# Optimization experiments

Hardware: AMD Instinct MI355X
Metric: run time of the kernel (lower is better)

## Reference

```python
import jax, jax.numpy as jnp
import numpy as np
from jax import lax

# 5x5 ring kernel: all ones except center (same_class_neighbor in the torch code)
_RING = np.ones((5, 5), dtype=np.float32)
_RING[2, 2] = 0.0


def _ring_dwconv(x, channels):
    """Depthwise 5x5 'ring' conv, padding=2 (groups=channels in torch)."""
    k = jnp.broadcast_to(jnp.asarray(_RING)[None, None], (channels, 1, 5, 5))
    return lax.conv_general_dilated(
        x, k, window_strides=(1, 1), padding='SAME',
        dimension_numbers=('NCHW', 'OIHW', 'NCHW'),
        feature_group_count=channels)


def _gt2boundary(gt, ignore_label=-1, bw=5):
    # gt: [B,H,W] int. Differences over a width-5 offset, padded back to size.
    ud = jnp.pad(gt[:, bw:, :] - gt[:, :-bw, :], ((0, 0), (0, bw), (0, 0))) != 0
    lr = jnp.pad(gt[:, :, bw:] - gt[:, :, :-bw], ((0, 0), (0, 0), (0, bw))) != 0
    return ud | lr | (gt == ignore_label)


def setup_inputs() -> dict:
    key = jax.random.key(0)
    k1, k2, k3 = jax.random.split(key, 3)
    B, C, H, W, NC = 4, 256, 256, 256, 2
    out_features = jax.random.normal(k1, (B, C, H, W), dtype=jnp.float32)
    out_classifier = jax.random.normal(k2, (B, NC, H, W), dtype=jnp.float32)
    gt_sem = jax.random.randint(k3, (B, H, W), 0, 2)
    return {"out_features": out_features, "out_classifier": out_classifier, "gt_sem": gt_sem}


def reference(out_features, out_classifier, gt_sem):
    NUM_CLASSES = 2
    B, C, H, W = out_features.shape
    # boundary mask (gt2boundary); interpolation to er_input size is identity here
    edge = _gt2boundary(gt_sem)  # [B,H,W] bool
    pred = jnp.argmax(out_classifier, axis=1)  # [B,H,W]

    total = jnp.float32(0.0)
    ncls = jnp.float32(0.0)
    for c in range(NUM_CLASSES):
        cm = (gt_sem == c).astype(out_features.dtype)   # now_class_mask
        pm = (pred == c).astype(out_features.dtype)     # now_pred_class_mask
        corr = cm * pm                                   # correctly-predicted class mask
        # depthwise ring-neighborhood sums
        neigh_feat = _ring_dwconv(out_features * corr[:, None], C)      # [B,C,H,W]
        cnt_class = _ring_dwconv(cm[:, None], 1)[:, 0]                  # [B,H,W]
        cnt_corr = _ring_dwconv(corr[:, None], 1)[:, 0]                 # [B,H,W]
        cal_mask = (cnt_class >= 1) & edge & (cm > 0)
        mse_mask = (cnt_corr >= 1) & edge & (cm > 0) & (pm > 0)
        # mean neighbor feature of correctly-predicted same-class neighbors
        feat = neigh_feat / (cnt_corr[:, None] + 1e-5)
        m = mse_mask.astype(out_features.dtype)
        nsel = jnp.sum(m)
        diff = (out_features - lax.stop_gradient(feat)) * m[:, None]
        # F.mse_loss(reduction='mean') over selected pixels x C channels
        loss_c = jnp.sum(diff * diff) / jnp.maximum(nsel * C, 1.0)
        valid = (jnp.sum(cal_mask) >= 1) & (jnp.sum(mse_mask) >= 1)
        total = total + jnp.where(valid, loss_c, 0.0)
        ncls = ncls + valid.astype(jnp.float32)
    # if no class contributed, return 0 (the unaveraged total); else average
    return jnp.where(ncls == 0, total, total / jnp.maximum(ncls, 1.0))
```

## Files before the change

kernel.cpp:

```cpp
#include <hip/hip_runtime.h>
#include <stdint.h>

#define BB 4
#define CC 256
#define HH 256
#define WW 256
#define TH 16
#define TR 20
#define NCH 8
#define NTILES (HH/TH)
#define NCHUNKS (CC/NCH)

__global__ void k_init(unsigned int* p) {
    if (threadIdx.x < 8) p[threadIdx.x] = 0;
}

__global__ void k_code(const float* __restrict__ cls, const int* __restrict__ gt,
                       unsigned char* __restrict__ code) {
    int i = blockIdx.x * 256 + threadIdx.x;
    int w = i & 255, h = (i >> 8) & 255;
    int b = i >> 16;
    int g = gt[i];
    float c0 = cls[((b*2 + 0)*HH + h)*WW + w];
    float c1 = cls[((b*2 + 1)*HH + h)*WW + w];
    int pred = (c1 > c0) ? 1 : 0;
    int ud = (h < HH-5) ? (gt[i + 5*WW] != g) : 0;
    int lr = (w < WW-5) ? (gt[i + 5] != g) : 0;
    int edge = (ud | lr | (g == -1)) ? 1 : 0;
    int lab = (g == 0) ? 0 : ((g == 1) ? 1 : 2);
    int good = (lab < 2 && pred == g) ? 1 : 0;
    code[i] = (unsigned char)(lab | (good << 2) | (edge << 3));
}

__device__ __forceinline__ float f4get(const float4& v, int j) {
    switch (j) { case 0: return v.x; case 1: return v.y; case 2: return v.z; default: return v.w; }
}

__device__ __forceinline__ void hwin_f(const float* vs, float* S, int l) {
    float eL0 = __shfl(vs[2], l - 1, 64);
    float eL1 = __shfl(vs[3], l - 1, 64);
    float eR0 = __shfl(vs[0], l + 1, 64);
    float eR1 = __shfl(vs[1], l + 1, 64);
    if (l == 0)  { eL0 = 0.f; eL1 = 0.f; }
    if (l == 63) { eR0 = 0.f; eR1 = 0.f; }
    float m = vs[1] + vs[2];
    float core = vs[0] + m;
    float c2 = m + vs[3];
    S[0] = core + eL0 + eL1;
    S[1] = core + vs[3] + eL1;
    S[2] = core + vs[3] + eR0;
    S[3] = c2 + eR0 + eR1;
}

__device__ __forceinline__ void hwin_i(const int* vs, int* S, int l) {
    int eL0 = __shfl(vs[2], l - 1, 64);
    int eL1 = __shfl(vs[3], l - 1, 64);
    int eR0 = __shfl(vs[0], l + 1, 64);
    int eR1 = __shfl(vs[1], l + 1, 64);
    if (l == 0)  { eL0 = 0; eL1 = 0; }
    if (l == 63) { eR0 = 0; eR1 = 0; }
    int m = vs[1] + vs[2];
    int core = vs[0] + m;
    int c2 = m + vs[3];
    S[0] = core + eL0 + eL1;
    S[1] = core + vs[3] + eL1;
    S[2] = core + vs[3] + eR0;
    S[3] = c2 + eR0 + eR1;
}

__global__ __launch_bounds__(256) void k_loss(const float* __restrict__ F,
                                              const unsigned char* __restrict__ code,
                                              double* __restrict__ lsum,
                                              unsigned int* __restrict__ cnts) {
    __shared__ unsigned int csh[TR*64];
    __shared__ float red[8];
    const int t = threadIdx.x, w = t >> 6, l = t & 63;
    const int bx = blockIdx.x;
    const int chunk = bx & (NCHUNKS - 1);
    const int tile = (bx >> 5) & (NTILES - 1);
    const int b = bx >> 9;
    const int R0 = tile * TH;

    for (int idx = t; idx < TR*64; idx += 256) {
        int rr = idx >> 6, grow = R0 - 2 + rr;
        unsigned int v = 0x02020202u;
        if ((unsigned)grow < HH) v = ((const unsigned int*)code)[(b*HH + grow)*64 + (idx & 63)];
        csh[idx] = v;
    }
    __syncthreads();

    const int rbase = R0 + 4*w - 2;

    unsigned int cw[8];
    #pragma unroll
    for (int rr = 0; rr < 8; rr++) cw[rr] = csh[(4*w + rr)*64 + l];

    float fm0[8][4], fm1[8][4];
    unsigned int mgd[8], mcls[8];
    #pragma unroll
    for (int rr = 0; rr < 8; rr++) {
        unsigned int u = cw[rr], mg = 0, mc = 0;
        #pragma unroll
        for (int j = 0; j < 4; j++) {
            unsigned int q = (u >> (8*j)) & 255u;
            unsigned int lab2 = q & 3u, good = (q >> 2) & 1u;
            unsigned int c0 = (lab2 == 0u) ? 1u : 0u;
            unsigned int c1 = (lab2 == 1u) ? 1u : 0u;
            mg |= (c0 & good) << j;
            mg |= (c1 & good) << (4 + j);
            mc |= c0 << j;
            mc |= c1 << (4 + j);
            fm0[rr][j] = (float)(c0 & good);
            fm1[rr][j] = (float)(c1 & good);
        }
        mgd[rr] = mg; mcls[rr] = mc;
    }

    float wq[16];
    unsigned int mse0bits = 0, mse1bits = 0, labbits = 0;
    int ccal0 = 0, ccal1 = 0, cms0 = 0, cms1 = 0;
    #pragma unroll
    for (int o = 0; o < 4; o++) {
        int vg0[4] = {0,0,0,0}, vg1[4] = {0,0,0,0}, vc0[4] = {0,0,0,0}, vc1[4] = {0,0,0,0};
        #pragma unroll
        for (int k = 0; k < 5; k++) {
            unsigned int mg = mgd[o+k], mc = mcls[o+k];
            #pragma unroll
            for (int j = 0; j < 4; j++) {
                vg0[j] += (mg >> j) & 1;  vg1[j] += (mg >> (4+j)) & 1;
                vc0[j] += (mc >> j) & 1;  vc1[j] += (mc >> (4+j)) & 1;
            }
        }
        int bg0[4], bg1[4], bc0[4], bc1[4];
        hwin_i(vg0, bg0, l); hwin_i(vg1, bg1, l);
        hwin_i(vc0, bc0, l); hwin_i(vc1, bc1, l);
        #pragma unroll
        for (int j = 0; j < 4; j++) {
            unsigned int q = (cw[o+2] >> (8*j)) & 255u;
            int lab2 = q & 3, good = (q >> 2) & 1, edge = (q >> 3) & 1;
            int bcl = (lab2 == 1) ? bc1[j] : bc0[j];
            int bgl = (lab2 == 1) ? bg1[j] : bg0[j];
            int ccls = bcl - 1;
            int ccorr = bgl - good;
            int isc = (lab2 < 2) && edge;
            int cal = isc && (ccls >= 1);
            int mse = isc && good && (ccorr >= 1);
            int idx = o*4 + j;
            wq[idx] = mse ? (1.0f / ((float)ccorr + 1e-5f)) : 0.0f;
            labbits  |= ((unsigned)(lab2 & 1)) << idx;
            mse0bits |= ((unsigned)(mse & (lab2 == 0))) << idx;
            mse1bits |= ((unsigned)(mse & (lab2 == 1))) << idx;
            ccal0 += cal & (lab2 == 0);  ccal1 += cal & (lab2 == 1);
            cms0  += mse & (lab2 == 0);  cms1  += mse & (lab2 == 1);
        }
    }

    if (chunk == 0) {
        for (int off = 32; off > 0; off >>= 1) {
            ccal0 += __shfl_down(ccal0, off, 64);
            ccal1 += __shfl_down(ccal1, off, 64);
            cms0  += __shfl_down(cms0,  off, 64);
            cms1  += __shfl_down(cms1,  off, 64);
        }
        if (l == 0) {
            atomicAdd(&cnts[0], (unsigned)ccal0);
            atomicAdd(&cnts[1], (unsigned)ccal1);
            atomicAdd(&cnts[2], (unsigned)cms0);
            atomicAdd(&cnts[3], (unsigned)cms1);
        }
    }

    unsigned int rowok = 0;
    #pragma unroll
    for (int rr = 0; rr < 8; rr++)
        if ((unsigned)(rbase + rr) < HH) rowok |= 1u << rr;

    const float4* fb = (const float4*)F + (((size_t)(b*CC + chunk*NCH)) << 14);
    float acc0 = 0.f, acc1 = 0.f;

    #pragma unroll 1
    for (int c = 0; c < NCH; c++) {
        const float4* pl = fb + ((size_t)c << 14);
        float4 ring[5];
        #pragma unroll
        for (int rr = 0; rr < 8; rr++) {
            float4 v = make_float4(0.f, 0.f, 0.f, 0.f);
            if (rowok & (1u << rr)) v = pl[(rbase + rr)*64 + l];
            ring[rr % 5] = v;
            if (rr >= 4) {
                const int o = rr - 4;
                float vs0[4] = {0.f,0.f,0.f,0.f}, vs1[4] = {0.f,0.f,0.f,0.f};
                #pragma unroll
                for (int k = 0; k < 5; k++) {
                    const int row = o + k;
                    const float4 rv = ring[row % 5];
                    #pragma unroll
                    for (int j = 0; j < 4; j++) {
                        float x = f4get(rv, j);
                        vs0[j] = fmaf(fm0[row][j], x, vs0[j]);
                        vs1[j] = fmaf(fm1[row][j], x, vs1[j]);
                    }
                }
                float S0[4], S1[4];
                hwin_f(vs0, S0, l);
                hwin_f(vs1, S1, l);
                const float4 ctr = ring[(o + 2) % 5];
                #pragma unroll
                for (int j = 0; j < 4; j++) {
                    const int idx = o*4 + j;
                    float fc = f4get(ctr, j);
                    float Ssel = ((labbits >> idx) & 1u) ? S1[j] : S0[j];
                    float S = Ssel - fc;
                    float d = fmaf(-S, wq[idx], fc);
                    float dd = d * d;
                    acc0 += ((mse0bits >> idx) & 1u) ? dd : 0.f;
                    acc1 += ((mse1bits >> idx) & 1u) ? dd : 0.f;
                }
            }
        }
    }

    for (int off = 32; off > 0; off >>= 1) {
        acc0 += __shfl_down(acc0, off, 64);
        acc1 += __shfl_down(acc1, off, 64);
    }
    if (l == 0) { red[w*2] = acc0; red[w*2 + 1] = acc1; }
    __syncthreads();
    if (t == 0) {
        float a0 = red[0] + red[2] + red[4] + red[6];
        float a1 = red[1] + red[3] + red[5] + red[7];
        atomicAdd(&lsum[0], (double)a0);
        atomicAdd(&lsum[1], (double)a1);
    }
}

__global__ void k_final(const double* __restrict__ lsum,
                        const unsigned int* __restrict__ cnts, float* out) {
    if (threadIdx.x == 0 && blockIdx.x == 0) {
        float total = 0.f, ncls = 0.f;
        for (int c = 0; c < 2; c++) {
            double num = lsum[c];
            unsigned int calc = cnts[c], msec = cnts[2 + c];
            float denom = fmaxf((float)msec * (float)CC, 1.0f);
            float lc = (float)(num / (double)denom);
            if (calc >= 1u && msec >= 1u) { total += lc; ncls += 1.f; }
        }
        out[0] = (ncls == 0.f) ? total : total / fmaxf(ncls, 1.f);
    }
}

extern "C" void kernel_launch(void* const* d_in, const int* in_sizes, int n_in,
                              void* d_out, int out_size, void* d_ws, size_t ws_size,
                              hipStream_t stream) {
    const float* feats = (const float*)d_in[0];
    const float* cls   = (const float*)d_in[1];
    const int*   gt    = (const int*)d_in[2];
    double* lsum = (double*)d_ws;
    unsigned int* cnts = (unsigned int*)((char*)d_ws + 16);
    unsigned char* code = (unsigned char*)d_ws + 64;
    float* out = (float*)d_out;

    const int npix = BB*HH*WW;
    k_init<<<1, 64, 0, stream>>>((unsigned int*)d_ws);
    k_code<<<npix/256, 256, 0, stream>>>(cls, gt, code);
    k_loss<<<BB*NTILES*NCHUNKS, 256, 0, stream>>>(feats, code, lsum, cnts);
    k_final<<<1, 64, 0, stream>>>(lsum, cnts, out);
}
```

Before: 444.1 us.

## Double-buffer channel row loads and use DPP row shifts for horizontal window

The channel loop now prefetches the next channel's 8 rows into a second register buffer while the current one is computed, so global load latency overlaps compute. Cross-lane neighbor exchange switches from __shfl to DPP wave_shl/wave_shr with bound_ctrl zero-fill, which removes the ds_bpermute and the edge-lane masking. Launch bounds now request 3 waves per SIMD, and fewer code words are kept in registers. The extra float4 buffers raise register pressure, which may cause spills or lower occupancy.

```diff
diff --git a/kernel.cpp b/kernel.cpp
--- a/kernel.cpp
+++ b/kernel.cpp
@@ -32,17 +32,30 @@
     code[i] = (unsigned char)(lab | (good << 2) | (edge << 3));
 }
 
+__device__ __forceinline__ float dpp_from_left(float x) {
+    int r = __builtin_amdgcn_update_dpp(0, __builtin_bit_cast(int, x), 0x138, 0xf, 0xf, true);
+    return __builtin_bit_cast(float, r);
+}
+__device__ __forceinline__ float dpp_from_right(float x) {
+    int r = __builtin_amdgcn_update_dpp(0, __builtin_bit_cast(int, x), 0x130, 0xf, 0xf, true);
+    return __builtin_bit_cast(float, r);
+}
+__device__ __forceinline__ int dpp_from_left_i(int x) {
+    return __builtin_amdgcn_update_dpp(0, x, 0x138, 0xf, 0xf, true);
+}
+__device__ __forceinline__ int dpp_from_right_i(int x) {
+    return __builtin_amdgcn_update_dpp(0, x, 0x130, 0xf, 0xf, true);
+}
+
 __device__ __forceinline__ float f4get(const float4& v, int j) {
     switch (j) { case 0: return v.x; case 1: return v.y; case 2: return v.z; default: return v.w; }
 }
 
-__device__ __forceinline__ void hwin_f(const float* vs, float* S, int l) {
-    float eL0 = __shfl(vs[2], l - 1, 64);
-    float eL1 = __shfl(vs[3], l - 1, 64);
-    float eR0 = __shfl(vs[0], l + 1, 64);
-    float eR1 = __shfl(vs[1], l + 1, 64);
-    if (l == 0)  { eL0 = 0.f; eL1 = 0.f; }
-    if (l == 63) { eR0 = 0.f; eR1 = 0.f; }
+__device__ __forceinline__ void hwin_f(const float* vs, float* S) {
+    float eL0 = dpp_from_left(vs[2]);
+    float eL1 = dpp_from_left(vs[3]);
+    float eR0 = dpp_from_right(vs[0]);
+    float eR1 = dpp_from_right(vs[1]);
     float m = vs[1] + vs[2];
     float core = vs[0] + m;
     float c2 = m + vs[3];
@@ -52,13 +65,11 @@
     S[3] = c2 + eR0 + eR1;
 }
 
-__device__ __forceinline__ void hwin_i(const int* vs, int* S, int l) {
-    int eL0 = __shfl(vs[2], l - 1, 64);
-    int eL1 = __shfl(vs[3], l - 1, 64);
-    int eR0 = __shfl(vs[0], l + 1, 64);
-    int eR1 = __shfl(vs[1], l + 1, 64);
-    if (l == 0)  { eL0 = 0; eL1 = 0; }
-    if (l == 63) { eR0 = 0; eR1 = 0; }
+__device__ __forceinline__ void hwin_i(const int* vs, int* S) {
+    int eL0 = dpp_from_left_i(vs[2]);
+    int eL1 = dpp_from_left_i(vs[3]);
+    int eR0 = dpp_from_right_i(vs[0]);
+    int eR1 = dpp_from_right_i(vs[1]);
     int m = vs[1] + vs[2];
     int core = vs[0] + m;
     int c2 = m + vs[3];
@@ -68,10 +79,10 @@
     S[3] = c2 + eR0 + eR1;
 }
 
-__global__ __launch_bounds__(256) void k_loss(const float* __restrict__ F,
-                                              const unsigned char* __restrict__ code,
-                                              double* __restrict__ lsum,
-                                              unsigned int* __restrict__ cnts) {
+__global__ __launch_bounds__(256, 3) void k_loss(const float* __restrict__ F,
+                                                 const unsigned char* __restrict__ code,
+                                                 double* __restrict__ lsum,
+                                                 unsigned int* __restrict__ cnts) {
     __shared__ unsigned int csh[TR*64];
     __shared__ float red[8];
     const int t = threadIdx.x, w = t >> 6, l = t & 63;
@@ -91,15 +102,13 @@
 
     const int rbase = R0 + 4*w - 2;
 
-    unsigned int cw[8];
-    #pragma unroll
-    for (int rr = 0; rr < 8; rr++) cw[rr] = csh[(4*w + rr)*64 + l];
-
     float fm0[8][4], fm1[8][4];
     unsigned int mgd[8], mcls[8];
+    unsigned int cw2[4];
     #pragma unroll
     for (int rr = 0; rr < 8; rr++) {
-        unsigned int u = cw[rr], mg = 0, mc = 0;
+        unsigned int u = csh[(4*w + rr)*64 + l];
+        unsigned int mg = 0, mc = 0;
         #pragma unroll
         for (int j = 0; j < 4; j++) {
             unsigned int q = (u >> (8*j)) & 255u;
@@ -114,6 +123,7 @@
             fm1[rr][j] = (float)(c1 & good);
         }
         mgd[rr] = mg; mcls[rr] = mc;
+        if (rr >= 2 && rr <= 5) cw2[rr - 2] = u;
     }
 
     float wq[16];
@@ -132,11 +142,11 @@
             }
         }
         int bg0[4], bg1[4], bc0[4], bc1[4];
-        hwin_i(vg0, bg0, l); hwin_i(vg1, bg1, l);
-        hwin_i(vc0, bc0, l); hwin_i(vc1, bc1, l);
+        hwin_i(vg0, bg0); hwin_i(vg1, bg1);
+        hwin_i(vc0, bc0); hwin_i(vc1, bc1);
         #pragma unroll
         for (int j = 0; j < 4; j++) {
-            unsigned int q = (cw[o+2] >> (8*j)) & 255u;
+            unsigned int q = (cw2[o] >> (8*j)) & 255u;
             int lab2 = q & 3, good = (q >> 2) & 1, edge = (q >> 3) & 1;
             int bcl = (lab2 == 1) ? bc1[j] : bc0[j];
             int bgl = (lab2 == 1) ? bg1[j] : bg0[j];
@@ -178,47 +188,63 @@
     const float4* fb = (const float4*)F + (((size_t)(b*CC + chunk*NCH)) << 14);
     float acc0 = 0.f, acc1 = 0.f;
 
+    float4 Areg[8], Breg[8];
+
+    #define LOADROWS(dst, ci)                                                    \
+        {                                                                        \
+            const float4* pl = fb + ((size_t)(ci) << 14);                        \
+            _Pragma("unroll")                                                    \
+            for (int rr = 0; rr < 8; rr++) {                                     \
+                float4 v = make_float4(0.f, 0.f, 0.f, 0.f);                      \
+                if (rowok & (1u << rr)) v = pl[(rbase + rr)*64 + l];             \
+                dst[rr] = v;                                                     \
+            }                                                                    \
+        }
+
+    #define COMPUTE(src)                                                         \
+        {                                                                        \
+            _Pragma("unroll")                                                    \
+            for (int o = 0; o < 4; o++) {                                        \
+                float vs0[4] = {0.f,0.f,0.f,0.f}, vs1[4] = {0.f,0.f,0.f,0.f};    \
+                _Pragma("unroll")                                                \
+                for (int k = 0; k < 5; k++) {                                    \
+                    const int row = o + k;                                       \
+                    const float4 rv = src[row];                                  \
+                    _Pragma("unroll")                                            \
+                    for (int j = 0; j < 4; j++) {                                \
+                        float x = f4get(rv, j);                                  \
+                        vs0[j] = fmaf(fm0[row][j], x, vs0[j]);                   \
+                        vs1[j] = fmaf(fm1[row][j], x, vs1[j]);                   \
+                    }                                                            \
+                }                                                                \
+                float S0[4], S1[4];                                              \
+                hwin_f(vs0, S0);                                                 \
+                hwin_f(vs1, S1);                                                 \
+                const float4 ctr = src[o + 2];                                   \
+                _Pragma("unroll")                                                \
+                for (int j = 0; j < 4; j++) {                                    \
+                    const int idx = o*4 + j;                                     \
+                    float fc = f4get(ctr, j);                                    \
+                    float Ssel = ((labbits >> idx) & 1u) ? S1[j] : S0[j];        \
+                    float S = Ssel - fc;                                         \
+                    float d = fmaf(-S, wq[idx], fc);                             \
+                    float dd = d * d;                                            \
+                    acc0 += ((mse0bits >> idx) & 1u) ? dd : 0.f;                 \
+                    acc1 += ((mse1bits >> idx) & 1u) ? dd : 0.f;                 \
+                }                                                                \
+            }                                                                    \
+        }
+
+    LOADROWS(Areg, 0);
     #pragma unroll 1
-    for (int c = 0; c < NCH; c++) {
-        const float4* pl = fb + ((size_t)c << 14);
-        float4 ring[5];
-        #pragma unroll
-        for (int rr = 0; rr < 8; rr++) {
-            float4 v = make_float4(0.f, 0.f, 0.f, 0.f);
-            if (rowok & (1u << rr)) v = pl[(rbase + rr)*64 + l];
-            ring[rr % 5] = v;
-            if (rr >= 4) {
-                const int o = rr - 4;
-                float vs0[4] = {0.f,0.f,0.f,0.f}, vs1[4] = {0.f,0.f,0.f,0.f};
-                #pragma unroll
-                for (int k = 0; k < 5; k++) {
-                    const int row = o + k;
-                    const float4 rv = ring[row % 5];
-                    #pragma unroll
-                    for (int j = 0; j < 4; j++) {
-                        float x = f4get(rv, j);
-                        vs0[j] = fmaf(fm0[row][j], x, vs0[j]);
-                        vs1[j] = fmaf(fm1[row][j], x, vs1[j]);
-                    }
-                }
-                float S0[4], S1[4];
-                hwin_f(vs0, S0, l);
-                hwin_f(vs1, S1, l);
-                const float4 ctr = ring[(o + 2) % 5];
-                #pragma unroll
-                for (int j = 0; j < 4; j++) {
-                    const int idx = o*4 + j;
-                    float fc = f4get(ctr, j);
-                    float Ssel = ((labbits >> idx) & 1u) ? S1[j] : S0[j];
-                    float S = Ssel - fc;
-                    float d = fmaf(-S, wq[idx], fc);
-                    float dd = d * d;
-                    acc0 += ((mse0bits >> idx) & 1u) ? dd : 0.f;
-                    acc1 += ((mse1bits >> idx) & 1u) ? dd : 0.f;
-                }
-            }
-        }
-    }
+    for (int c = 0; c < NCH; c += 2) {
+        LOADROWS(Breg, c + 1);
+        COMPUTE(Areg);
+        if (c + 2 < NCH) LOADROWS(Areg, c + 2);
+        COMPUTE(Breg);
+    }
+    #undef LOADROWS
+    #undef COMPUTE
 
     for (int off = 32; off > 0; off >>= 1) {
         acc0 += __shfl_down(acc0, off, 64);
```

Result: slower. 623.3 us (+40.3%).
